# Kernel tuning notes

Measured on AMD Instinct MI355X. Metric: run time of the kernel, lower is better.

The kernel has to match this reference:

```python
import jax, jax.numpy as jnp
import numpy as np

P = 17  # prediction chunk size
H = 50  # hidden size

def _lstm_cell(x, h, c, Wih, Whh, bih, bhh):
    # torch LSTMCell: gates = x@Wih^T + bih + h@Whh^T + bhh, order i,f,g,o
    g = x @ Wih.T + h @ Whh.T + (bih + bhh)
    i, f, gg, o = jnp.split(g, 4, axis=-1)
    c_new = jax.nn.sigmoid(f) * c + jax.nn.sigmoid(i) * jnp.tanh(gg)
    h_new = jax.nn.sigmoid(o) * jnp.tanh(c_new)
    return h_new, c_new

def setup_inputs() -> dict:
    key = jax.random.key(0)
    ks = jax.random.split(key, 16)
    B, T = 2048, 512
    s = 1.0 / np.sqrt(H)
    u = lambda k, shp: jax.random.uniform(k, shp, jnp.float32, -s, s)
    return {
        "x": jax.random.normal(ks[0], (B, T * P), jnp.float32),
        "W_ih1": u(ks[1], (4 * H, P)),  "W_hh1": u(ks[2], (4 * H, H)),
        "b_ih1": u(ks[3], (4 * H,)),    "b_hh1": u(ks[4], (4 * H,)),
        "W_ih2": u(ks[5], (4 * H, H)),  "W_hh2": u(ks[6], (4 * H, H)),
        "b_ih2": u(ks[7], (4 * H,)),    "b_hh2": u(ks[8], (4 * H,)),
        "W_ih3": u(ks[9], (4 * H, H)),  "W_hh3": u(ks[10], (4 * H, H)),
        "b_ih3": u(ks[11], (4 * H,)),   "b_hh3": u(ks[12], (4 * H,)),
        "W_lin": u(ks[13], (P, H)),     "b_lin": u(ks[14], (P,)),
        "future": 544,
    }

def reference(x, W_ih1, W_hh1, b_ih1, b_hh1, W_ih2, W_hh2, b_ih2, b_hh2,
              W_ih3, W_hh3, b_ih3, b_hh3, W_lin, b_lin, future):
    B = x.shape[0]
    T = x.shape[1] // P
    xs = x.reshape(B, T, P).transpose(1, 0, 2)  # [T, B, P]
    z = jnp.zeros((B, H), jnp.float32)
    init = (z, z, z, z, z, z)

    def cell_stack(state, inp):
        h1, c1, h2, c2, h3, c3 = state
        h1, c1 = _lstm_cell(inp, h1, c1, W_ih1, W_hh1, b_ih1, b_hh1)
        h2, c2 = _lstm_cell(h1, h2, c2, W_ih2, W_hh2, b_ih2, b_hh2)
        h3, c3 = _lstm_cell(h2, h3, c3, W_ih3, W_hh3, b_ih3, b_hh3)
        out = h3 @ W_lin.T + b_lin  # [B, P]
        return (h1, c1, h2, c2, h3, c3), out

    def step(state, xt):
        return cell_stack(state, xt)

    state, outs = jax.lax.scan(step, init, xs)  # outs: [T, B, P]

    n_future = int(future) // P
    if n_future > 0:
        last = outs[-1]

        def fstep(carry, _):
            state, out = carry
            state, out = cell_stack(state, out)
            return (state, out), out

        _, fouts = jax.lax.scan(fstep, (state, last), None, length=n_future)
        outs = jnp.concatenate([outs, fouts], axis=0)  # [T+next, B, P]

    return outs.transpose(1, 0, 2).reshape(B, -1)  # [B, (T+next)*P]
```

## Files before the change

kernel.cpp:

```cpp
#include <hip/hip_runtime.h>
#include <math.h>


#define BATCH    2048
#define PP       17
#define HH       50
#define GG       200
#define MROWS    8
#define NTHREADS 512
#define NBLOCKS  (BATCH / MROWS)

__device__ __forceinline__ float bf2f(unsigned short u) {
    unsigned int i = ((unsigned int)u) << 16;
    float f; __builtin_memcpy(&f, &i, 4); return f;
}
__device__ __forceinline__ unsigned short f2bf(float f) {
    unsigned int i; __builtin_memcpy(&i, &f, 4);
    return (unsigned short)((i + 0x7fffu + ((i >> 16) & 1u)) >> 16);
}
__device__ __forceinline__ float ldin(const void* p, long i, bool f32) {
    return f32 ? ((const float*)p)[i] : bf2f(((const unsigned short*)p)[i]);
}
__device__ __forceinline__ float fsig(float x) {
    float t = exp2f(-1.44269504089f * x);
    return __builtin_amdgcn_rcpf(1.0f + t);
}
__device__ __forceinline__ float ftanh(float x) {
    float t = exp2f(2.88539008178f * x);
    return 1.0f - 2.0f * __builtin_amdgcn_rcpf(t + 1.0f);
}

extern "C" __global__ void sniff_dtype(const unsigned short* __restrict__ w,
                                       int* __restrict__ flag) {
    int lane = threadIdx.x;
    bool bad = false;
#pragma unroll
    for (int t = 0; t < 4; ++t) {
        float v = bf2f(w[lane * 4 + t]);
        bad |= !(fabsf(v) <= 1.0f);
    }
    unsigned long long m = __ballot(bad);
    if (lane == 0) flag[0] = (m != 0ULL) ? 1 : 0;
}

template <int TQ>
__device__ __forceinline__ void gate_phase(const float* __restrict__ S,
                                           float* __restrict__ gb,
                                           const float w[2][TQ],
                                           int srow, int g2, int q, bool active) {
    if (active) {
        float aA[8] = {0, 0, 0, 0, 0, 0, 0, 0};
        float aB[8] = {0, 0, 0, 0, 0, 0, 0, 0};
        const float4* Sp = (const float4*)(S + (srow + q * TQ) * MROWS);
#pragma unroll
        for (int t = 0; t < TQ; ++t) {
            float wa = w[0][t], wb = w[1][t];
            float4 lo = Sp[2 * t];
            float4 hi = Sp[2 * t + 1];
            aA[0] = fmaf(wa, lo.x, aA[0]); aA[1] = fmaf(wa, lo.y, aA[1]);
            aA[2] = fmaf(wa, lo.z, aA[2]); aA[3] = fmaf(wa, lo.w, aA[3]);
            aA[4] = fmaf(wa, hi.x, aA[4]); aA[5] = fmaf(wa, hi.y, aA[5]);
            aA[6] = fmaf(wa, hi.z, aA[6]); aA[7] = fmaf(wa, hi.w, aA[7]);
            aB[0] = fmaf(wb, lo.x, aB[0]); aB[1] = fmaf(wb, lo.y, aB[1]);
            aB[2] = fmaf(wb, lo.z, aB[2]); aB[3] = fmaf(wb, lo.w, aB[3]);
            aB[4] = fmaf(wb, hi.x, aB[4]); aB[5] = fmaf(wb, hi.y, aB[5]);
            aB[6] = fmaf(wb, hi.z, aB[6]); aB[7] = fmaf(wb, hi.w, aB[7]);
        }
#pragma unroll
        for (int m = 0; m < 8; ++m) {
            float2 v; v.x = aA[m]; v.y = aB[m];
            ((float2*)(gb + (q * MROWS + m) * GG))[g2] = v;
        }
    }
}

__device__ __forceinline__ void lstm_update(float* __restrict__ S,
                                            const float* __restrict__ gb,
                                            const float* __restrict__ bs,
                                            float& c, int hrow, int tid) {
    int m = tid & 7;
    int j = tid >> 3;
    float ii = bs[j], ff = bs[50 + j], gg = bs[100 + j], oo = bs[150 + j];
#pragma unroll
    for (int q = 0; q < 4; ++q) {
        const float* b = gb + (q * MROWS + m) * GG;
        ii += b[j]; ff += b[50 + j]; gg += b[100 + j]; oo += b[150 + j];
    }
    float cn = fsig(ff) * c + fsig(ii) * ftanh(gg);
    c = cn;
    S[(hrow + j) * MROWS + m] = fsig(oo) * ftanh(cn);
}

extern "C" __global__ void __launch_bounds__(NTHREADS, 2)
lstm_persistent(const void* __restrict__ x,
                const void* __restrict__ wih1, const void* __restrict__ whh1,
                const void* __restrict__ bih1, const void* __restrict__ bhh1,
                const void* __restrict__ wih2, const void* __restrict__ whh2,
                const void* __restrict__ bih2, const void* __restrict__ bhh2,
                const void* __restrict__ wih3, const void* __restrict__ whh3,
                const void* __restrict__ bih3, const void* __restrict__ bhh3,
                const void* __restrict__ wlin, const void* __restrict__ blin,
                void* __restrict__ out, const int* __restrict__ flag,
                int T, int steps)
{
    const int tid = threadIdx.x;
    __shared__ float S[167 * MROWS];
    __shared__ float gb[4 * MROWS * GG];
    __shared__ float WLt[50 * PP];
    __shared__ float bs1[GG], bs2[GG], bs3[GG], bl[PP];

    const bool f32 = (flag[0] != 0);

    const int q  = tid >> 7;
    const int g2 = tid & 127;
    const bool active = (g2 < 100);

    float w1[2][17], w2[2][25], w3[2][25];
    if (active) {
#pragma unroll
        for (int e = 0; e < 2; ++e) {
            const int g = 2 * g2 + e;
#pragma unroll
            for (int t = 0; t < 17; ++t) {
                int k = q * 17 + t;
                w1[e][t] = (k < 17) ? ldin(wih1, (long)g * 17 + k, f32)
                         : (k < 67) ? ldin(whh1, (long)g * 50 + (k - 17), f32)
                                    : 0.0f;
            }
#pragma unroll
            for (int t = 0; t < 25; ++t) {
                int k = q * 25 + t;
                w2[e][t] = (k < 50) ? ldin(wih2, (long)g * 50 + k, f32)
                                    : ldin(whh2, (long)g * 50 + (k - 50), f32);
            }
#pragma unroll
            for (int t = 0; t < 25; ++t) {
                int k = q * 25 + t;
                w3[e][t] = (k < 50) ? ldin(wih3, (long)g * 50 + k, f32)
                                    : ldin(whh3, (long)g * 50 + (k - 50), f32);
            }
        }
    }

    if (tid < GG) {
        bs1[tid] = ldin(bih1, tid, f32) + ldin(bhh1, tid, f32);
        bs2[tid] = ldin(bih2, tid, f32) + ldin(bhh2, tid, f32);
        bs3[tid] = ldin(bih3, tid, f32) + ldin(bhh3, tid, f32);
    } else if (tid < GG + PP) {
        bl[tid - GG] = ldin(blin, tid - GG, f32);
    }
    for (int i = tid; i < 50 * PP; i += NTHREADS) {
        int k = i / PP, p = i - k * PP;
        WLt[i] = ldin(wlin, (long)p * 50 + k, f32);
    }
    for (int i = tid; i < 1200; i += NTHREADS) S[136 + i] = 0.0f;

    const long rowBase = (long)blockIdx.x * MROWS;
    const long xStride = (long)T * PP;
    if (tid < 136) {
        int m = tid / PP, p = tid - (tid / PP) * PP;
        S[p * MROWS + m] = ldin(x, (rowBase + m) * xStride + p, f32);
    }
    float c1 = 0.0f, c2 = 0.0f, c3 = 0.0f;
    __syncthreads();

    const long outStride = (long)steps * PP;
    for (int s = 0; s < steps; ++s) {
        gate_phase<17>(S, gb, w1, 0, g2, q, active);
        __syncthreads();
        if (tid < 400) lstm_update(S, gb, bs1, c1, 17, tid);
        __syncthreads();
        gate_phase<25>(S, gb, w2, 17, g2, q, active);
        __syncthreads();
        if (tid < 400) lstm_update(S, gb, bs2, c2, 67, tid);
        __syncthreads();
        gate_phase<25>(S, gb, w3, 67, g2, q, active);
        __syncthreads();
        if (tid < 400) lstm_update(S, gb, bs3, c3, 117, tid);
        __syncthreads();
        if (tid < 136) {
            int m = tid / PP, p = tid - (tid / PP) * PP;
            float acc = bl[p];
#pragma unroll
            for (int k = 0; k < 50; ++k)
                acc = fmaf(WLt[k * PP + p], S[(117 + k) * MROWS + m], acc);
            long oi = (rowBase + m) * outStride + (long)s * PP + p;
            if (f32) ((float*)out)[oi] = acc;
            else     ((unsigned short*)out)[oi] = f2bf(acc);
            if (s + 1 >= T && s + 1 < steps)
                S[p * MROWS + m] = acc;
        } else if (tid >= 256 && tid < 392) {
            int u = tid - 256;
            int m = u / PP, p = u - (u / PP) * PP;
            if (s + 1 < T)
                S[p * MROWS + m] = ldin(x, (rowBase + m) * xStride + (long)(s + 1) * PP + p, f32);
        }
        __syncthreads();
    }
}

extern "C" void kernel_launch(void* const* d_in, const int* in_sizes, int n_in,
                              void* d_out, int out_size, void* d_ws, size_t ws_size,
                              hipStream_t stream) {
    (void)ws_size; (void)n_in;
    int* flag = (int*)d_ws;

    const int T     = in_sizes[0] / (BATCH * PP);
    const int steps = out_size / (BATCH * PP);

    sniff_dtype<<<1, 64, 0, stream>>>((const unsigned short*)d_in[1], flag);

    lstm_persistent<<<NBLOCKS, NTHREADS, 0, stream>>>(
        d_in[0],
        d_in[1], d_in[2], d_in[3], d_in[4],
        d_in[5], d_in[6], d_in[7], d_in[8],
        d_in[9], d_in[10], d_in[11], d_in[12],
        d_in[13], d_in[14],
        d_out, flag, T, steps);
}
```

Measured before the change: 3.823 ms.

## Assign one gate per thread with five-way K split over 1024 threads

Result: slower. 8.203 ms (+114.6%).

```diff
diff --git a/kernel.cpp b/kernel.cpp
--- a/kernel.cpp
+++ b/kernel.cpp
@@ -7,8 +7,12 @@
 #define HH       50
 #define GG       200
 #define MROWS    8
-#define NTHREADS 512
+#define NQ       5
+#define NTHREADS 1024
 #define NBLOCKS  (BATCH / MROWS)
+#define TQ1      14
+#define TQ2      20
+#define TQ3      20
 
 __device__ __forceinline__ float bf2f(unsigned short u) {
     unsigned int i = ((unsigned int)u) << 16;
@@ -46,31 +50,24 @@
 template <int TQ>
 __device__ __forceinline__ void gate_phase(const float* __restrict__ S,
                                            float* __restrict__ gb,
-                                           const float w[2][TQ],
-                                           int srow, int g2, int q, bool active) {
+                                           const float w[TQ],
+                                           int srow, int g, int q, bool active) {
     if (active) {
-        float aA[8] = {0, 0, 0, 0, 0, 0, 0, 0};
-        float aB[8] = {0, 0, 0, 0, 0, 0, 0, 0};
+        float a[8] = {0, 0, 0, 0, 0, 0, 0, 0};
         const float4* Sp = (const float4*)(S + (srow + q * TQ) * MROWS);
 #pragma unroll
         for (int t = 0; t < TQ; ++t) {
-            float wa = w[0][t], wb = w[1][t];
+            float wv = w[t];
             float4 lo = Sp[2 * t];
             float4 hi = Sp[2 * t + 1];
-            aA[0] = fmaf(wa, lo.x, aA[0]); aA[1] = fmaf(wa, lo.y, aA[1]);
-            aA[2] = fmaf(wa, lo.z, aA[2]); aA[3] = fmaf(wa, lo.w, aA[3]);
-            aA[4] = fmaf(wa, hi.x, aA[4]); aA[5] = fmaf(wa, hi.y, aA[5]);
-            aA[6] = fmaf(wa, hi.z, aA[6]); aA[7] = fmaf(wa, hi.w, aA[7]);
-            aB[0] = fmaf(wb, lo.x, aB[0]); aB[1] = fmaf(wb, lo.y, aB[1]);
-            aB[2] = fmaf(wb, lo.z, aB[2]); aB[3] = fmaf(wb, lo.w, aB[3]);
-            aB[4] = fmaf(wb, hi.x, aB[4]); aB[5] = fmaf(wb, hi.y, aB[5]);
-            aB[6] = fmaf(wb, hi.z, aB[6]); aB[7] = fmaf(wb, hi.w, aB[7]);
-        }
-#pragma unroll
-        for (int m = 0; m < 8; ++m) {
-            float2 v; v.x = aA[m]; v.y = aB[m];
-            ((float2*)(gb + (q * MROWS + m) * GG))[g2] = v;
-        }
+            a[0] = fmaf(wv, lo.x, a[0]); a[1] = fmaf(wv, lo.y, a[1]);
+            a[2] = fmaf(wv, lo.z, a[2]); a[3] = fmaf(wv, lo.w, a[3]);
+            a[4] = fmaf(wv, hi.x, a[4]); a[5] = fmaf(wv, hi.y, a[5]);
+            a[6] = fmaf(wv, hi.z, a[6]); a[7] = fmaf(wv, hi.w, a[7]);
+        }
+        float4* d = (float4*)(gb + (q * GG + g) * MROWS);
+        d[0] = make_float4(a[0], a[1], a[2], a[3]);
+        d[1] = make_float4(a[4], a[5], a[6], a[7]);
     }
 }
 
@@ -82,16 +79,17 @@
     int j = tid >> 3;
     float ii = bs[j], ff = bs[50 + j], gg = bs[100 + j], oo = bs[150 + j];
 #pragma unroll
-    for (int q = 0; q < 4; ++q) {
-        const float* b = gb + (q * MROWS + m) * GG;
-        ii += b[j]; ff += b[50 + j]; gg += b[100 + j]; oo += b[150 + j];
+    for (int q = 0; q < NQ; ++q) {
+        const float* b = gb + q * (GG * MROWS) + m;
+        ii += b[j * 8]; ff += b[(50 + j) * 8];
+        gg += b[(100 + j) * 8]; oo += b[(150 + j) * 8];
     }
     float cn = fsig(ff) * c + fsig(ii) * ftanh(gg);
     c = cn;
     S[(hrow + j) * MROWS + m] = fsig(oo) * ftanh(cn);
 }
 
-extern "C" __global__ void __launch_bounds__(NTHREADS, 2)
+extern "C" __global__ void __launch_bounds__(NTHREADS, 4)
 lstm_persistent(const void* __restrict__ x,
                 const void* __restrict__ wih1, const void* __restrict__ whh1,
                 const void* __restrict__ bih1, const void* __restrict__ bhh1,
@@ -105,40 +103,36 @@
 {
     const int tid = threadIdx.x;
     __shared__ float S[167 * MROWS];
-    __shared__ float gb[4 * MROWS * GG];
+    __shared__ float gb[NQ * GG * MROWS];
     __shared__ float WLt[50 * PP];
     __shared__ float bs1[GG], bs2[GG], bs3[GG], bl[PP];
 
     const bool f32 = (flag[0] != 0);
 
-    const int q  = tid >> 7;
-    const int g2 = tid & 127;
-    const bool active = (g2 < 100);
-
-    float w1[2][17], w2[2][25], w3[2][25];
+    const int q = tid / GG;
+    const int g = tid - q * GG;
+    const bool active = (tid < NQ * GG);
+
+    float w1[TQ1], w2[TQ2], w3[TQ3];
     if (active) {
 #pragma unroll
-        for (int e = 0; e < 2; ++e) {
-            const int g = 2 * g2 + e;
-#pragma unroll
-            for (int t = 0; t < 17; ++t) {
-                int k = q * 17 + t;
-                w1[e][t] = (k < 17) ? ldin(wih1, (long)g * 17 + k, f32)
-                         : (k < 67) ? ldin(whh1, (long)g * 50 + (k - 17), f32)
-                                    : 0.0f;
-            }
-#pragma unroll
-            for (int t = 0; t < 25; ++t) {
-                int k = q * 25 + t;
-                w2[e][t] = (k < 50) ? ldin(wih2, (long)g * 50 + k, f32)
-                                    : ldin(whh2, (long)g * 50 + (k - 50), f32);
-            }
-#pragma unroll
-            for (int t = 0; t < 25; ++t) {
-                int k = q * 25 + t;
-                w3[e][t] = (k < 50) ? ldin(wih3, (long)g * 50 + k, f32)
-                                    : ldin(whh3, (long)g * 50 + (k - 50), f32);
-            }
+        for (int t = 0; t < TQ1; ++t) {
+            int k = q * TQ1 + t;
+            w1[t] = (k < 17) ? ldin(wih1, (long)g * 17 + k, f32)
+                  : (k < 67) ? ldin(whh1, (long)g * 50 + (k - 17), f32)
+                             : 0.0f;
+        }
+#pragma unroll
+        for (int t = 0; t < TQ2; ++t) {
+            int k = q * TQ2 + t;
+            w2[t] = (k < 50) ? ldin(wih2, (long)g * 50 + k, f32)
+                             : ldin(whh2, (long)g * 50 + (k - 50), f32);
+        }
+#pragma unroll
+        for (int t = 0; t < TQ3; ++t) {
+            int k = q * TQ3 + t;
+            w3[t] = (k < 50) ? ldin(wih3, (long)g * 50 + k, f32)
+                             : ldin(whh3, (long)g * 50 + (k - 50), f32);
         }
     }
 
@@ -166,15 +160,15 @@
 
     const long outStride = (long)steps * PP;
     for (int s = 0; s < steps; ++s) {
-        gate_phase<17>(S, gb, w1, 0, g2, q, active);
+        gate_phase<TQ1>(S, gb, w1, 0, g, q, active);
         __syncthreads();
         if (tid < 400) lstm_update(S, gb, bs1, c1, 17, tid);
         __syncthreads();
-        gate_phase<25>(S, gb, w2, 17, g2, q, active);
+        gate_phase<TQ2>(S, gb, w2, 17, g, q, active);
         __syncthreads();
         if (tid < 400) lstm_update(S, gb, bs2, c2, 67, tid);
         __syncthreads();
-        gate_phase<25>(S, gb, w3, 67, g2, q, active);
+        gate_phase<TQ3>(S, gb, w3, 67, g, q, active);
         __syncthreads();
         if (tid < 400) lstm_update(S, gb, bs3, c3, 117, tid);
         __syncthreads();
```
